# Optimization experiments

Hardware: AMD Instinct MI355X
Metric: run time of the kernel (lower is better)

## Reference

```python
import jax, jax.numpy as jnp
import numpy as np

VOCAB = 50000
DIM = 768


def setup_inputs() -> dict:
    key = jax.random.key(0)
    k1, k2, k3, k4 = jax.random.split(key, 4)
    token = jax.random.randint(k1, (32, 512), 0, VOCAB, dtype=jnp.int64)
    need_mapper = jax.random.randint(k2, (VOCAB,), 0, 2, dtype=jnp.int32)
    bert_embedding = jax.random.normal(k3, (VOCAB, DIM), dtype=jnp.float32)
    mapper_w = jax.random.normal(k4, (DIM, DIM), dtype=jnp.float32) * (1.0 / np.sqrt(DIM))
    mapper_b = jnp.zeros((DIM,), dtype=jnp.float32)
    return {
        "token": token,
        "need_mapper": need_mapper,
        "bert_embedding": bert_embedding,
        "mapper_w": mapper_w,
        "mapper_b": mapper_b,
    }


def reference(token, need_mapper, bert_embedding, mapper_w, mapper_b):
    # Gather: [B, S, D] -- irregular access into the embedding table.
    vecs = bert_embedding[token]
    # Conditional mapper (vectorized over all tokens; selected by per-id mask).
    mapped = jnp.einsum("bsd,de->bse", vecs, mapper_w) + mapper_b
    need = need_mapper[token].astype(bool)  # [B, S]
    return jnp.where(need[..., None], mapped, vecs)
```

## Files before the change

### kernel.cpp

```cpp
#include <hip/hip_runtime.h>
#include <stdint.h>
#include <stddef.h>

#define DIM 768

typedef short short8 __attribute__((ext_vector_type(8)));
typedef float f32x4 __attribute__((ext_vector_type(4)));

__device__ inline unsigned short f2bf_rne(float f) {
    union { float f; unsigned u; } x; x.f = f;
    unsigned r = x.u + 0x7fffu + ((x.u >> 16) & 1u);
    return (unsigned short)(r >> 16);
}

__device__ inline void gload_lds16(const void* g, void* l) {
    __builtin_amdgcn_global_load_lds((const __attribute__((address_space(1))) void*)g,
                                     (__attribute__((address_space(3))) void*)l, 16, 0, 0);
}

__global__ __launch_bounds__(256) void convw_kernel(
    const float* __restrict__ w, unsigned short* __restrict__ Bt)
{
    __shared__ unsigned short t[64][65];
    const int k0 = blockIdx.x * 64, n0 = blockIdx.y * 64;
    const int tid = threadIdx.x;
#pragma unroll
    for (int p = 0; p < 16; ++p) {
        int e = p * 256 + tid;
        int r = e >> 6, c = e & 63;
        t[c][r] = f2bf_rne(w[(size_t)(k0 + r) * DIM + n0 + c]);
    }
    __syncthreads();
#pragma unroll
    for (int p = 0; p < 16; ++p) {
        int e = p * 256 + tid;
        int r = e >> 6, c = e & 63;
        Bt[(size_t)(n0 + r) * DIM + k0 + c] = t[r][c];
    }
}

__global__ __launch_bounds__(256) void fused_gemm_kernel(
    const int* __restrict__ token,
    const int* __restrict__ need_mapper,
    const float* __restrict__ emb,
    const unsigned short* __restrict__ Bt,
    const float* __restrict__ bias,
    float* __restrict__ out)
{
    const int cpx  = gridDim.x >> 3;
    const int orig = blockIdx.x;
    const int wgid = (orig & 7) * cpx + (orig >> 3);
    const int tile_m = wgid / 6;
    const int tile_n = wgid - tile_m * 6;

    __shared__ float          As[2][128 * 32];
    __shared__ unsigned short Bs[2][128 * 32];
    __shared__ int tok_s[128];
    __shared__ int flag_s[128];

    const int tid  = threadIdx.x;
    const int wave = tid >> 6;
    const int lane = tid & 63;
    const int quad = lane >> 4;
    const int l15  = lane & 15;
    const int wm   = wave >> 1;
    const int wn   = wave & 1;

    if (tid < 128) {
        int t = token[tile_m * 128 + tid];
        tok_s[tid]  = t;
        flag_s[tid] = need_mapper[t];
    }
    __syncthreads();

    const int r8 = tid >> 3;
    const int c8 = tid & 7;
    const float* pA[4];
#pragma unroll
    for (int j = 0; j < 4; ++j) {
        int r = j * 32 + r8;
        pA[j] = emb + (size_t)tok_s[r] * DIM + ((c8 ^ (r & 7)) << 2);
    }
    const int rb = tid >> 2;
    const int sb = tid & 3;
    const unsigned short* pB0 = Bt + (size_t)(tile_n * 128 + rb) * DIM + ((sb ^ ((rb >> 1) & 3)) << 3);
    const unsigned short* pB1 = Bt + (size_t)(tile_n * 128 + 64 + rb) * DIM + ((sb ^ (((64 + rb) >> 1) & 3)) << 3);

#define STAGE(b, kk) do { \
    _Pragma("unroll") \
    for (int j = 0; j < 4; ++j) \
        gload_lds16(pA[j] + (kk), &As[(b)][wave * 256 + j * 1024]); \
    gload_lds16(pB0 + (kk), &Bs[(b)][wave * 512]); \
    gload_lds16(pB1 + (kk), &Bs[(b)][2048 + wave * 512]); \
} while (0)

    f32x4 acc[4][4] = {};

#define COMPUTE(b) do { \
    short8 af[4], bf[4]; \
    _Pragma("unroll") \
    for (int i = 0; i < 4; ++i) { \
        const int m = wm * 64 + i * 16 + l15; \
        const float* row = &As[(b)][m << 5]; \
        f32x4 a0 = *(const f32x4*)(row + ((((quad << 1)    ) ^ (m & 7)) << 2)); \
        f32x4 a1 = *(const f32x4*)(row + ((((quad << 1) + 1) ^ (m & 7)) << 2)); \
        unsigned u0 = __float_as_uint(a0[0]) + 0x8000u; \
        unsigned u1 = __float_as_uint(a0[1]) + 0x8000u; \
        unsigned u2 = __float_as_uint(a0[2]) + 0x8000u; \
        unsigned u3 = __float_as_uint(a0[3]) + 0x8000u; \
        unsigned u4 = __float_as_uint(a1[0]) + 0x8000u; \
        unsigned u5 = __float_as_uint(a1[1]) + 0x8000u; \
        unsigned u6 = __float_as_uint(a1[2]) + 0x8000u; \
        unsigned u7 = __float_as_uint(a1[3]) + 0x8000u; \
        union { int i4[4]; short8 s; } pk; \
        pk.i4[0] = __builtin_amdgcn_perm(u1, u0, 0x07060302); \
        pk.i4[1] = __builtin_amdgcn_perm(u3, u2, 0x07060302); \
        pk.i4[2] = __builtin_amdgcn_perm(u5, u4, 0x07060302); \
        pk.i4[3] = __builtin_amdgcn_perm(u7, u6, 0x07060302); \
        af[i] = pk.s; \
    } \
    _Pragma("unroll") \
    for (int j = 0; j < 4; ++j) { \
        const int n = wn * 64 + j * 16 + l15; \
        bf[j] = *(const short8*)(&Bs[(b)][n * 32 + ((quad ^ ((n >> 1) & 3)) << 3)]); \
    } \
    _Pragma("unroll") \
    for (int i = 0; i < 4; ++i) \
        _Pragma("unroll") \
        for (int j = 0; j < 4; ++j) \
            acc[i][j] = __builtin_amdgcn_mfma_f32_16x16x32_bf16(af[i], bf[j], acc[i][j], 0, 0, 0); \
} while (0)

    STAGE(0, 0);
    __syncthreads();
    int cur = 0;
    for (int kk = 32; kk < DIM; kk += 32) {
        STAGE(cur ^ 1, kk);
        COMPUTE(cur);
        __syncthreads();
        cur ^= 1;
    }
    COMPUTE(cur);

    const int colg = tile_n * 128 + wn * 64 + l15;
    float bv[4];
#pragma unroll
    for (int j = 0; j < 4; ++j) bv[j] = bias[colg + j * 16];

#pragma unroll
    for (int i = 0; i < 4; ++i) {
#pragma unroll
        for (int r = 0; r < 4; ++r) {
            const int lrow = wm * 64 + i * 16 + quad * 4 + r;
            const int gm   = tile_m * 128 + lrow;
            float* orow = out + (size_t)gm * DIM + colg;
            if (flag_s[lrow]) {
#pragma unroll
                for (int j = 0; j < 4; ++j)
                    orow[j * 16] = acc[i][j][r] + bv[j];
            } else {
                const float* erow = emb + (size_t)tok_s[lrow] * DIM + colg;
#pragma unroll
                for (int j = 0; j < 4; ++j)
                    orow[j * 16] = erow[j * 16];
            }
        }
    }
#undef STAGE
#undef COMPUTE
}

extern "C" void kernel_launch(void* const* d_in, const int* in_sizes, int n_in,
                              void* d_out, int out_size, void* d_ws, size_t ws_size,
                              hipStream_t stream)
{
    const int*   token       = (const int*)d_in[0];
    const int*   need_mapper = (const int*)d_in[1];
    const float* emb         = (const float*)d_in[2];
    const float* w           = (const float*)d_in[3];
    const float* bias        = (const float*)d_in[4];
    float* out = (float*)d_out;

    const int ntok = in_sizes[0];

    unsigned short* Bt = (unsigned short*)d_ws;

    convw_kernel<<<dim3(DIM / 64, DIM / 64), dim3(256), 0, stream>>>(w, Bt);
    fused_gemm_kernel<<<dim3((ntok / 128) * 6), dim3(256), 0, stream>>>(
        token, need_mapper, emb, Bt, bias, out);
}
```

Measured before the change: 285.7 us.

## Relax pipeline barriers, drop B swizzle, and use a 2D grid

Replaces the __syncthreads around the double-buffered K loop with explicit vmcnt/lgkmcnt waits and raw s_barrier, so the next stage's global-to-LDS loads stay in flight during compute. It also removes the XOR swizzle on the B tile in LDS and the XCD-aware block remapping, launching a plain 2D grid instead. The unswizzled B reads may cause LDS bank conflicts, and losing the XCD remap may reduce L2 reuse of embedding rows across N tiles.

Result: faster. 244.6 us (-14.4%).

```diff
diff --git a/kernel.cpp b/kernel.cpp
--- a/kernel.cpp
+++ b/kernel.cpp
@@ -47,12 +47,6 @@
     const float* __restrict__ bias,
     float* __restrict__ out)
 {
-    const int cpx  = gridDim.x >> 3;
-    const int orig = blockIdx.x;
-    const int wgid = (orig & 7) * cpx + (orig >> 3);
-    const int tile_m = wgid / 6;
-    const int tile_n = wgid - tile_m * 6;
-
     __shared__ float          As[2][128 * 32];
     __shared__ unsigned short Bs[2][128 * 32];
     __shared__ int tok_s[128];
@@ -65,6 +59,8 @@
     const int l15  = lane & 15;
     const int wm   = wave >> 1;
     const int wn   = wave & 1;
+    const int tile_m = blockIdx.x;
+    const int tile_n = blockIdx.y;
 
     if (tid < 128) {
         int t = token[tile_m * 128 + tid];
@@ -81,17 +77,14 @@
         int r = j * 32 + r8;
         pA[j] = emb + (size_t)tok_s[r] * DIM + ((c8 ^ (r & 7)) << 2);
     }
-    const int rb = tid >> 2;
-    const int sb = tid & 3;
-    const unsigned short* pB0 = Bt + (size_t)(tile_n * 128 + rb) * DIM + ((sb ^ ((rb >> 1) & 3)) << 3);
-    const unsigned short* pB1 = Bt + (size_t)(tile_n * 128 + 64 + rb) * DIM + ((sb ^ (((64 + rb) >> 1) & 3)) << 3);
+    const unsigned short* pB = Bt + (size_t)(tile_n * 128 + (tid >> 2)) * DIM + (tid & 3) * 8;
 
 #define STAGE(b, kk) do { \
     _Pragma("unroll") \
     for (int j = 0; j < 4; ++j) \
-        gload_lds16(pA[j] + (kk), &As[(b)][wave * 256 + j * 1024]); \
-    gload_lds16(pB0 + (kk), &Bs[(b)][wave * 512]); \
-    gload_lds16(pB1 + (kk), &Bs[(b)][2048 + wave * 512]); \
+        gload_lds16(pA[j] + (kk), &As[(b)][(wave * 8) * 32 + j * 32 * 32]); \
+    gload_lds16(pB + (kk),                   &Bs[(b)][wave * 512]); \
+    gload_lds16(pB + (kk) + (size_t)64 * DIM, &Bs[(b)][2048 + wave * 512]); \
 } while (0)
 
     f32x4 acc[4][4] = {};
@@ -120,10 +113,8 @@
         af[i] = pk.s; \
     } \
     _Pragma("unroll") \
-    for (int j = 0; j < 4; ++j) { \
-        const int n = wn * 64 + j * 16 + l15; \
-        bf[j] = *(const short8*)(&Bs[(b)][n * 32 + ((quad ^ ((n >> 1) & 3)) << 3)]); \
-    } \
+    for (int j = 0; j < 4; ++j) \
+        bf[j] = *(const short8*)(&Bs[(b)][(wn * 64 + j * 16 + l15) * 32 + quad * 8]); \
     _Pragma("unroll") \
     for (int i = 0; i < 4; ++i) \
         _Pragma("unroll") \
@@ -132,14 +123,21 @@
 } while (0)
 
     STAGE(0, 0);
-    __syncthreads();
     int cur = 0;
     for (int kk = 32; kk < DIM; kk += 32) {
         STAGE(cur ^ 1, kk);
+        asm volatile("s_waitcnt vmcnt(6)" ::: "memory");
+        __builtin_amdgcn_sched_barrier(0);
+        __builtin_amdgcn_s_barrier();
         COMPUTE(cur);
-        __syncthreads();
+        asm volatile("s_waitcnt lgkmcnt(0)" ::: "memory");
+        __builtin_amdgcn_sched_barrier(0);
+        __builtin_amdgcn_s_barrier();
         cur ^= 1;
     }
+    asm volatile("s_waitcnt vmcnt(0)" ::: "memory");
+    __builtin_amdgcn_sched_barrier(0);
+    __builtin_amdgcn_s_barrier();
     COMPUTE(cur);
 
     const int colg = tile_n * 128 + wn * 64 + l15;
@@ -186,6 +184,6 @@
     unsigned short* Bt = (unsigned short*)d_ws;
 
     convw_kernel<<<dim3(DIM / 64, DIM / 64), dim3(256), 0, stream>>>(w, Bt);
-    fused_gemm_kernel<<<dim3((ntok / 128) * 6), dim3(256), 0, stream>>>(
+    fused_gemm_kernel<<<dim3(ntok / 128, DIM / 128), dim3(256), 0, stream>>>(
         token, need_mapper, emb, Bt, bias, out);
 }
```
